# Performance work log

Measured on AMD Instinct MI355X. Metric: run time of the kernel, lower is better.

Reference implementation:

```python
import jax, jax.numpy as jnp
import numpy as np

T, B, I, H = 129, 1024, 512, 2048


def setup_inputs() -> dict:
    key = jax.random.key(0)
    ks = jax.random.split(key, 12)
    s = 1.0 / np.sqrt(H)  # torch RNNCell/Linear default U(-1/sqrt(H), 1/sqrt(H))

    def u(k, shape):
        return jax.random.uniform(k, shape, jnp.float32, -s, s)

    x = jax.random.normal(ks[0], (T, B, I), jnp.float32)
    return {
        "x": x,
        "enc_Wih": u(ks[1], (H, I)), "enc_Whh": u(ks[2], (H, H)),
        "enc_bih": u(ks[3], (H,)),   "enc_bhh": u(ks[4], (H,)),
        "dec_Wih": u(ks[5], (H, I)), "dec_Whh": u(ks[6], (H, H)),
        "dec_bih": u(ks[7], (H,)),   "dec_bhh": u(ks[8], (H,)),
        "ro_W": u(ks[9], (I, H)),    "ro_b": u(ks[10], (I,)),
    }


def reference(x, enc_Wih, enc_Whh, enc_bih, enc_bhh,
              dec_Wih, dec_Whh, dec_bih, dec_bhh, ro_W, ro_b):
    T_, B_, I_ = x.shape
    H_ = enc_Whh.shape[0]
    k = (T_ - 3) // 2

    # ---- encode: k+2 RNNCell steps over x[0:k+2] ----
    def enc_step(h, xt):
        h = jnp.tanh(xt @ enc_Wih.T + enc_bih + h @ enc_Whh.T + enc_bhh)
        return h, None

    h0 = jnp.zeros((B_, H_), x.dtype)
    h, _ = jax.lax.scan(enc_step, h0, x[:k + 2])

    # begin_char: one-hot at index 0 (also the default fill of `outputs`)
    begin = jnp.zeros((B_, I_), x.dtype).at[:, 0].set(1.0)

    # ---- decode: k+1 steps, input is zeros (so zeros @ dec_Wih == 0) ----
    def dec_step(carry, _):
        h, done = carry
        h = jnp.tanh(dec_bih + h @ dec_Whh.T + dec_bhh)
        out = jax.nn.log_softmax(h @ ro_W.T + ro_b, axis=1)  # [B, I]
        z = (jnp.argmax(out, axis=1) == 2).astype(x.dtype)
        done = jnp.maximum(done, z)
        b = done[:, None]
        o = (1.0 - b) * out + b * begin
        return (h, done), o

    done0 = jnp.zeros((B_,), x.dtype)
    (_, _), outputs = jax.lax.scan(dec_step, (h, done0), None, length=k + 1)
    return outputs  # [k+1, B, I]
```

## Files before the change

kernel.cpp:

```cpp
#include <hip/hip_runtime.h>
#include <math.h>

constexpr int Bsz  = 1024;
constexpr int Isz  = 512;
constexpr int Hsz  = 2048;
constexpr int Tenc = 65;
constexpr int Tdec = 64;
constexpr int BI   = Bsz * Isz;
constexpr int MNh  = Bsz * Hsz;

typedef _Float16 half8 __attribute__((ext_vector_type(8)));
typedef float    f32x4 __attribute__((ext_vector_type(4)));
typedef unsigned int uint;
typedef unsigned short ushort;

__device__ inline uint pack_split(float v) {
    _Float16 a0 = (_Float16)v;
    float r = (v - (float)a0) * 4096.f;
    _Float16 a1 = (_Float16)r;
    return ((uint)__builtin_bit_cast(ushort, a1) << 16) | __builtin_bit_cast(ushort, a0);
}
__device__ inline void split_pair(float v0, float v1, uint& lo, uint& hi) {
    _Float16 a0 = (_Float16)v0, a1 = (_Float16)v1;
    _Float16 b0 = (_Float16)((v0 - (float)a0) * 4096.f);
    _Float16 b1 = (_Float16)((v1 - (float)a1) * 4096.f);
    lo = (uint)__builtin_bit_cast(ushort, a0) | ((uint)__builtin_bit_cast(ushort, a1) << 16);
    hi = (uint)__builtin_bit_cast(ushort, b0) | ((uint)__builtin_bit_cast(ushort, b1) << 16);
}

struct U8 { uint4 a, b; };
__device__ inline U8 ld8(const uint* __restrict__ p) {
    U8 r; r.a = *(const uint4*)p; r.b = *(const uint4*)(p + 4); return r;
}

__device__ inline void split8(const U8& v, half8& lo, half8& hi) {
    union { uint4 u; float f[4]; } A, B;
    A.u = v.a; B.u = v.b;
    float x[8] = {A.f[0], A.f[1], A.f[2], A.f[3], B.f[0], B.f[1], B.f[2], B.f[3]};
#pragma unroll
    for (int e = 0; e < 8; ++e) {
        _Float16 a0 = (_Float16)x[e];
        float r = (x[e] - (float)a0) * 4096.f;
        lo[e] = a0; hi[e] = (_Float16)r;
    }
}
__device__ inline void unpack8(const U8& v, half8& lo, half8& hi) {
    union { uint u[4]; half8 h; } L, H;
    uint w[8] = {v.a.x, v.a.y, v.a.z, v.a.w, v.b.x, v.b.y, v.b.z, v.b.w};
#pragma unroll
    for (int q = 0; q < 4; ++q) {
        L.u[q] = __builtin_amdgcn_perm(w[2*q+1], w[2*q], 0x05040100u);
        H.u[q] = __builtin_amdgcn_perm(w[2*q+1], w[2*q], 0x07060302u);
    }
    lo = L.h; hi = H.h;
}

__device__ __forceinline__ void gll16(const uint* g, uint* l) {
    __builtin_amdgcn_global_load_lds(
        (const __attribute__((address_space(1))) void*)(uintptr_t)g,
        (__attribute__((address_space(3))) void*)(unsigned int)(uintptr_t)l,
        16, 0, 0);
}

__device__ __forceinline__ void gemm_body(
    uint* ldsA, uint* ldsB,
    const uint* A1, int K1, const uint* B1,
    const uint* A2, int K2, const uint* B2,
    float* P, int M, int N, int GM, int GN, int KS, int bid)
{
    constexpr int NV = 8;
    const int tid  = threadIdx.x;
    const int wid  = tid >> 6, lane = tid & 63;
    const int wr   = wid >> 1, wc = wid & 1;
    const int kq   = lane >> 4, lr = lane & 15;

    const int xcd = bid & 7, g = bid >> 3;
    int n_b, m_b, ks;
    const int spx = GN >> 3;
    if (spx > 0) {
        n_b = xcd * spx + (g % spx);
        int r = g / spx; m_b = r % GM; ks = r / GM;
    } else {
        const int xpn = 8 / GN;
        n_b = xcd / xpn;
        int r = g * xpn + (xcd % xpn); m_b = r % GM; ks = r / GM;
    }
    const int m0 = m_b * 128, n0 = n_b * 128;

    int offA1[4], offA2[4], offB1[4], offB2[4];
#pragma unroll
    for (int q = 0; q < 4; ++q) {
        int U = q * 256 + tid, row = U >> 3, us = U & 7;
        int u = us ^ (row & 7);
        offA1[q] = (m0 + row) * K1 + u * 4;
        offA2[q] = (m0 + row) * K2 + u * 4;
        offB1[q] = (n0 + row) * K1 + u * 4;
        offB2[q] = (n0 + row) * K2 + u * 4;
    }
    const int ldsbase = wid * 256;

    const int R1 = K1 / 32;
    const int R  = (K1 + K2) / 32;
    const int nr = R / KS;
    const int r0 = ks * nr;

    auto STAGE = [&](int r, int bi) {
        uint* Ab = ldsA + bi * 4096;
        uint* Bb = ldsB + bi * 4096;
        const bool ph1 = r < R1;
        const int kl = (ph1 ? r : r - R1) * 32;
        const uint* As = ph1 ? A1 : A2;
        const uint* Bs = ph1 ? B1 : B2;
#pragma unroll
        for (int q = 0; q < 4; ++q)
            gll16(As + (ph1 ? offA1[q] : offA2[q]) + kl, Ab + q * 1024 + ldsbase);
#pragma unroll
        for (int q = 0; q < 4; ++q)
            gll16(Bs + (ph1 ? offB1[q] : offB2[q]) + kl, Bb + q * 1024 + ldsbase);
    };

    f32x4 acc0[4][4] = {}; f32x4 acc1[4][4] = {};

    auto FRAG = [&](const uint* buf, int row, half8& lo, half8& hi) {
        const int b = row * 8, s = row & 7;
        lo = *(const half8*)(buf + (b + (kq ^ s)) * 4);
        hi = *(const half8*)(buf + (b + ((kq + 4) ^ s)) * 4);
    };

    auto COMPUTE = [&](int bi) {
        const uint* Ab = ldsA + bi * 4096;
        const uint* Bb = ldsB + bi * 4096;
        half8 a0[4], a1[4];
#pragma unroll
        for (int i = 0; i < 4; ++i) FRAG(Ab, wr * 64 + i * 16 + lr, a0[i], a1[i]);
#pragma unroll
        for (int j = 0; j < 4; ++j) {
            half8 b0, b1;
            FRAG(Bb, wc * 64 + j * 16 + lr, b0, b1);
#pragma unroll
            for (int i = 0; i < 4; ++i) {
                acc0[i][j] = __builtin_amdgcn_mfma_f32_16x16x32_f16(a0[i], b0, acc0[i][j], 0, 0, 0);
                acc1[i][j] = __builtin_amdgcn_mfma_f32_16x16x32_f16(a1[i], b0, acc1[i][j], 0, 0, 0);
                acc1[i][j] = __builtin_amdgcn_mfma_f32_16x16x32_f16(a0[i], b1, acc1[i][j], 0, 0, 0);
            }
        }
    };

    STAGE(r0, 0);
    if (nr > 1) STAGE(r0 + 1, 1);
    __builtin_amdgcn_sched_barrier(0);
    if (nr > 1) asm volatile("s_waitcnt vmcnt(%0)" :: "i"(NV) : "memory");
    else        asm volatile("s_waitcnt vmcnt(0)"  ::: "memory");
    __builtin_amdgcn_s_barrier();
    __builtin_amdgcn_sched_barrier(0);

    int bi = 0;
    for (int t = 0; t < nr; ++t) {
        COMPUTE(bi);
        if (t + 1 < nr) {
            __builtin_amdgcn_sched_barrier(0);
            __builtin_amdgcn_s_barrier();
            __builtin_amdgcn_sched_barrier(0);
            if (t + 2 < nr) {
                STAGE(r0 + t + 2, bi);
                __builtin_amdgcn_sched_barrier(0);
                asm volatile("s_waitcnt vmcnt(%0)" :: "i"(NV) : "memory");
            } else {
                asm volatile("s_waitcnt vmcnt(0)" ::: "memory");
            }
            __builtin_amdgcn_s_barrier();
            __builtin_amdgcn_sched_barrier(0);
            bi ^= 1;
        }
    }

    float* Pk = P + (size_t)ks * M * N;
#pragma unroll
    for (int j = 0; j < 4; ++j) {
        const int n = n0 + wc * 64 + j * 16 + lr;
#pragma unroll
        for (int i = 0; i < 4; ++i) {
            const int mb = m0 + wr * 64 + i * 16 + kq * 4;
#pragma unroll
            for (int r = 0; r < 4; ++r)
                Pk[(size_t)(mb + r) * N + n] = acc0[i][j][r] + 0x1p-12f * acc1[i][j][r];
        }
    }
}

__global__ __launch_bounds__(256, 2) void gemm_pk4(
    const uint* __restrict__ A1, int K1, const uint* __restrict__ B1,
    const uint* __restrict__ A2, int K2, const uint* __restrict__ B2,
    float* __restrict__ P, int M, int N, int GM, int GN, int KS)
{
    __shared__ uint ldsA[2 * 4096];
    __shared__ uint ldsB[2 * 4096];
    gemm_body(ldsA, ldsB, A1, K1, B1, A2, K2, B2, P, M, N, GM, GN, KS, blockIdx.x);
}

__global__ __launch_bounds__(256, 2) void dec_work(
    const uint* __restrict__ hcur, const uint* __restrict__ pdWhh,
    const uint* __restrict__ proW,
    float* __restrict__ hparts, float* __restrict__ ropar, int doH)
{
    __shared__ uint ldsA[2 * 4096];
    __shared__ uint ldsB[2 * 4096];
    const int bid = blockIdx.x;
    if (bid < 512) {
        if (!doH) return;
        gemm_body(ldsA, ldsB, nullptr, 0, nullptr, hcur, Hsz, pdWhh,
                  hparts, Bsz, Hsz, 8, 16, 4, bid);
    } else {
        gemm_body(ldsA, ldsB, nullptr, 0, nullptr, hcur, Hsz, proW,
                  ropar, Bsz, Isz, 8, 4, 4, bid - 512);
    }
}

__device__ __forceinline__ void combine_dev(
    const float* __restrict__ P, const float* __restrict__ b1,
    const float* __restrict__ b2, uint* __restrict__ hout, int cb)
{
    const int i0 = (cb * 256 + threadIdx.x) * 8;
    float s[8];
#pragma unroll
    for (int e = 0; e < 8; ++e) s[e] = 0.f;
#pragma unroll
    for (int p = 0; p < 4; ++p) {
        float4 a = *(const float4*)(P + (size_t)p * MNh + i0);
        float4 b = *(const float4*)(P + (size_t)p * MNh + i0 + 4);
        s[0] += a.x; s[1] += a.y; s[2] += a.z; s[3] += a.w;
        s[4] += b.x; s[5] += b.y; s[6] += b.z; s[7] += b.w;
    }
    const int n = i0 & (Hsz - 1);
    float t[8];
#pragma unroll
    for (int e = 0; e < 8; ++e) t[e] = tanhf(s[e] + b1[n + e] + b2[n + e]);
    uint lo4[4], hi4[4];
#pragma unroll
    for (int q = 0; q < 4; ++q) split_pair(t[2*q], t[2*q+1], lo4[q], hi4[q]);
    uint* base = hout + ((i0 >> 5) << 5);
    const int eo = (i0 & 31) >> 1;
    *(uint4*)(base + eo)      = *(uint4*)lo4;
    *(uint4*)(base + 16 + eo) = *(uint4*)hi4;
}

__global__ __launch_bounds__(256) void combine_h4(
    const float* __restrict__ P, const float* __restrict__ b1,
    const float* __restrict__ b2, uint* __restrict__ hout)
{
    combine_dev(P, b1, b2, hout, blockIdx.x);
}

template<int NPART>
__device__ __forceinline__ void softmax_dev(
    const float* __restrict__ parts, const float* __restrict__ rob,
    float* __restrict__ done, float* __restrict__ out, int b)
{
    const int tid = threadIdx.x;
    const size_t S = (size_t)BI;
    const float* row = parts + (size_t)b * Isz;

    float v0, v1;
    if (NPART == 1) { v0 = row[tid]; v1 = row[tid + 256]; }
    else {
        v0 = rob[tid]; v1 = rob[tid + 256];
#pragma unroll
        for (int p = 0; p < NPART; ++p) { v0 += row[p*S + tid]; v1 += row[p*S + tid + 256]; }
    }

    float mv; int mi;
    if (v0 >= v1) { mv = v0; mi = tid; } else { mv = v1; mi = tid + 256; }
#pragma unroll
    for (int off = 32; off; off >>= 1) {
        float ov = __shfl_xor(mv, off);
        int   oi = __shfl_xor(mi, off);
        if (ov > mv || (ov == mv && oi < mi)) { mv = ov; mi = oi; }
    }
    __shared__ float smv[4];
    __shared__ int   smi[4];
    __shared__ float sdone;
    const int wid = tid >> 6, lane = tid & 63;
    if (lane == 0) { smv[wid] = mv; smi[wid] = mi; }
    __syncthreads();
    if (tid == 0) {
        for (int w = 1; w < 4; ++w)
            if (smv[w] > smv[0] || (smv[w] == smv[0] && smi[w] < smi[0])) {
                smv[0] = smv[w]; smi[0] = smi[w];
            }
        float z = (smi[0] == 2) ? 1.f : 0.f;
        float dn = fmaxf(done[b], z);
        done[b] = dn;
        sdone = dn;
    }
    __syncthreads();
    mv = smv[0];

    float s = expf(v0 - mv) + expf(v1 - mv);
#pragma unroll
    for (int off = 32; off; off >>= 1) s += __shfl_xor(s, off);
    __shared__ float ssum[4];
    if (lane == 0) ssum[wid] = s;
    __syncthreads();
    if (tid == 0) ssum[0] = ssum[0] + ssum[1] + ssum[2] + ssum[3];
    __syncthreads();
    const float ls = logf(ssum[0]);

    float* orow = out + (size_t)b * Isz;
    if (sdone > 0.5f) {
        orow[tid]       = (tid == 0) ? 1.f : 0.f;
        orow[tid + 256] = 0.f;
    } else {
        orow[tid]       = v0 - mv - ls;
        orow[tid + 256] = v1 - mv - ls;
    }
}

__global__ __launch_bounds__(256) void dec_fin(
    const float* __restrict__ hparts, const float* __restrict__ dbih,
    const float* __restrict__ dbhh, uint* __restrict__ hout,
    const float* __restrict__ ropar, const float* __restrict__ rob,
    float* __restrict__ done, float* __restrict__ out, int doH)
{
    const int bid = blockIdx.x;
    if (bid < 1024) {
        if (doH) combine_dev(hparts, dbih, dbhh, hout, bid);
    } else {
        softmax_dev<4>(ropar, rob, done, out, bid - 1024);
    }
}

__global__ __launch_bounds__(256) void logsoftmax_done1(
    const float* __restrict__ logits, const float* __restrict__ rob,
    float* __restrict__ done, float* __restrict__ out)
{
    softmax_dev<1>(logits, rob, done, out, blockIdx.x);
}

__global__ __launch_bounds__(256) void split_pack2_k(
    const float* __restrict__ s, uint* __restrict__ d, int n)
{
    for (int i = blockIdx.x * 256 + threadIdx.x; i < n; i += gridDim.x * 256) {
        const int c = i >> 5, j = i & 31;
        const int kb = c << 5;
        uint v;
        if (j < 16) {
            const int k = kb + (j << 1);
            _Float16 a0 = (_Float16)s[k], a1 = (_Float16)s[k + 1];
            v = (uint)__builtin_bit_cast(ushort, a0) |
                ((uint)__builtin_bit_cast(ushort, a1) << 16);
        } else {
            const int k = kb + ((j - 16) << 1);
            float f0 = s[k], f1 = s[k + 1];
            _Float16 b0 = (_Float16)((f0 - (float)(_Float16)f0) * 4096.f);
            _Float16 b1 = (_Float16)((f1 - (float)(_Float16)f1) * 4096.f);
            v = (uint)__builtin_bit_cast(ushort, b0) |
                ((uint)__builtin_bit_cast(ushort, b1) << 16);
        }
        d[i] = v;
    }
}

#define SWZ(row, kk) (((row) * 4 + ((kk) ^ (((row) >> 1) & 3))) * 8)

template<int BM, int BN, int WR, int WC, int MP, int NP, bool TANH, bool PACKOUT>
__global__ __launch_bounds__(WR*WC*64) void gemm_sp(
    const float* __restrict__ A1, int K1, const void* __restrict__ B1,
    const uint*  __restrict__ A2, int K2, const void* __restrict__ B2,
    int b_f32,
    const float* __restrict__ bias1, const float* __restrict__ bias2,
    void* __restrict__ C, int M, int N)
{
    constexpr int NT  = WR * WC * 64;
    constexpr int AUP = BM * 4 / NT;
    constexpr int BUP = BN * 4 / NT;

    __shared__ __align__(16) _Float16 As0[BM*32], As1[BM*32];
    __shared__ __align__(16) _Float16 Bs0[BN*32], Bs1[BN*32];

    const int tid  = threadIdx.x;
    const int wid  = tid >> 6, lane = tid & 63;
    const int wrow = wid / WC, wcol = wid % WC;
    const int kq   = lane >> 4, lr = lane & 15;
    const int m0   = blockIdx.y * BM;
    const int n0   = blockIdx.x * BN;

    int aum[AUP], auk[AUP]; _Float16 *aw0[AUP], *aw1[AUP];
#pragma unroll
    for (int p = 0; p < AUP; ++p) {
        int u = tid + p * NT; aum[p] = u >> 2; auk[p] = u & 3;
        int o = SWZ(aum[p], auk[p]); aw0[p] = As0 + o; aw1[p] = As1 + o;
    }
    int bun[BUP], buk[BUP]; _Float16 *bw0[BUP], *bw1[BUP];
#pragma unroll
    for (int p = 0; p < BUP; ++p) {
        int u = tid + p * NT; bun[p] = u >> 2; buk[p] = u & 3;
        int o = SWZ(bun[p], buk[p]); bw0[p] = Bs0 + o; bw1[p] = Bs1 + o;
    }
    int aoff[MP], boff[NP];
#pragma unroll
    for (int i = 0; i < MP; ++i) { int m = wrow*(MP*16) + i*16 + lr; aoff[i] = SWZ(m, kq); }
#pragma unroll
    for (int j = 0; j < NP; ++j) { int n = wcol*(NP*16) + j*16 + lr; boff[j] = SWZ(n, kq); }

    f32x4 acc0[MP][NP] = {}; f32x4 acc1[MP][NP] = {};

    const int R = (K1 + K2) / 32;

    auto issue = [&](int rd, U8* aR, U8* bR) {
        const bool ph1 = (rd * 32) < K1;
        const int  kl  = ph1 ? rd * 32 : rd * 32 - K1;
        const int  Ka  = ph1 ? K1 : K2;
        const uint* Ap = ph1 ? (const uint*)A1 : A2;
        const uint* Bp = (const uint*)(ph1 ? B1 : B2);
#pragma unroll
        for (int p = 0; p < AUP; ++p)
            aR[p] = ld8(Ap + (size_t)(m0 + aum[p]) * Ka + kl + auk[p] * 8);
#pragma unroll
        for (int p = 0; p < BUP; ++p)
            bR[p] = ld8(Bp + (size_t)(n0 + bun[p]) * Ka + kl + buk[p] * 8);
    };

    auto stage = [&](U8* aR, U8* bR, bool aF32) {
#pragma unroll
        for (int p = 0; p < AUP; ++p) {
            half8 lo, hi;
            if (aF32) split8(aR[p], lo, hi); else unpack8(aR[p], lo, hi);
            *(half8*)aw0[p] = lo; *(half8*)aw1[p] = hi;
        }
#pragma unroll
        for (int p = 0; p < BUP; ++p) {
            half8 lo, hi;
            if (b_f32) split8(bR[p], lo, hi); else unpack8(bR[p], lo, hi);
            *(half8*)bw0[p] = lo; *(half8*)bw1[p] = hi;
        }
    };

    auto compute = [&]() {
        half8 a0[MP], a1[MP], b0[NP], b1[NP];
#pragma unroll
        for (int i = 0; i < MP; ++i) {
            a0[i] = *(const half8*)(As0 + aoff[i]);
            a1[i] = *(const half8*)(As1 + aoff[i]);
        }
#pragma unroll
        for (int j = 0; j < NP; ++j) {
            b0[j] = *(const half8*)(Bs0 + boff[j]);
            b1[j] = *(const half8*)(Bs1 + boff[j]);
        }
#pragma unroll
        for (int i = 0; i < MP; ++i)
#pragma unroll
            for (int j = 0; j < NP; ++j) {
                acc0[i][j] = __builtin_amdgcn_mfma_f32_16x16x32_f16(a0[i], b0[j], acc0[i][j], 0, 0, 0);
                acc1[i][j] = __builtin_amdgcn_mfma_f32_16x16x32_f16(a1[i], b0[j], acc1[i][j], 0, 0, 0);
                acc1[i][j] = __builtin_amdgcn_mfma_f32_16x16x32_f16(a0[i], b1[j], acc1[i][j], 0, 0, 0);
            }
    };

    U8 aA[AUP], bA[BUP], aB[AUP], bB[BUP];
    issue(0, aA, bA);
    for (int rd = 0; rd < R; rd += 2) {
        if (rd + 1 < R) issue(rd + 1, aB, bB);
        stage(aA, bA, (rd * 32) < K1);
        __syncthreads();
        compute();
        __syncthreads();
        if (rd + 1 < R) {
            if (rd + 2 < R) issue(rd + 2, aA, bA);
            stage(aB, bB, ((rd + 1) * 32) < K1);
            __syncthreads();
            compute();
            __syncthreads();
        }
    }

#pragma unroll
    for (int j = 0; j < NP; ++j) {
        const int n = n0 + wcol*(NP*16) + j*16 + lr;
        float bb = bias1 ? bias1[n] : 0.f;
        if (bias2) bb += bias2[n];
#pragma unroll
        for (int i = 0; i < MP; ++i) {
            const int mb = m0 + wrow*(MP*16) + i*16 + kq*4;
#pragma unroll
            for (int r = 0; r < 4; ++r) {
                float val = acc0[i][j][r] + 0x1p-12f * acc1[i][j][r] + bb;
                if (TANH) val = tanhf(val);
                if (PACKOUT)
                    ((uint*)C)[(size_t)(mb + r) * N + n] = pack_split(val);
                else
                    ((float*)C)[(size_t)(mb + r) * N + n] = val;
            }
        }
    }
}

extern "C" void kernel_launch(void* const* d_in, const int* in_sizes, int n_in,
                              void* d_out, int out_size, void* d_ws, size_t ws_size,
                              hipStream_t stream)
{
    const float* x    = (const float*)d_in[0];
    const float* eWih = (const float*)d_in[1];
    const float* eWhh = (const float*)d_in[2];
    const float* ebih = (const float*)d_in[3];
    const float* ebhh = (const float*)d_in[4];
    const float* dWhh = (const float*)d_in[6];
    const float* dbih = (const float*)d_in[7];
    const float* dbhh = (const float*)d_in[8];
    const float* roW  = (const float*)d_in[9];
    const float* rob  = (const float*)d_in[10];
    float* out = (float*)d_out;

    const size_t sz_pWih = (size_t)Hsz * Isz * 4;
    const size_t sz_pWhh = (size_t)Hsz * Hsz * 4;
    const size_t sz_proW = (size_t)Isz * Hsz * 4;
    const size_t sz_h    = (size_t)MNh * 4;
    const size_t sz_hp   = (size_t)4 * MNh * 4;
    const size_t sz_rp   = (size_t)4 * BI * 4;
    const size_t sz_done = (size_t)Bsz * 4;
    const size_t sz_px2  = (size_t)Tenc * BI * 4;
    const size_t sz_slot = (size_t)BI * 4;

    const size_t base = sz_pWih + 2*sz_pWhh + sz_proW + 2*sz_h + sz_hp + sz_rp + sz_done;
    const int mode = (ws_size >= base + sz_px2) ? 2
                   : (ws_size >= base + sz_slot) ? 1 : 0;

    char* ws = (char*)d_ws;

    if (mode >= 1) {
        size_t off = 0;
        uint* pWih   = (uint*)(ws + off); off += sz_pWih;
        uint* pWhh   = (uint*)(ws + off); off += sz_pWhh;
        uint* pdWhh  = (uint*)(ws + off); off += sz_pWhh;
        uint* proW   = (uint*)(ws + off); off += sz_proW;
        uint* hA     = (uint*)(ws + off); off += sz_h;
        uint* hB     = (uint*)(ws + off); off += sz_h;
        float* hparts= (float*)(ws + off); off += sz_hp;
        float* ropar = (float*)(ws + off); off += sz_rp;
        float* done  = (float*)(ws + off); off += sz_done;
        uint* px     = (uint*)(ws + off);

        split_pack2_k<<<dim3(1024), dim3(256), 0, stream>>>(eWih, pWih,  Hsz*Isz);
        split_pack2_k<<<dim3(2048), dim3(256), 0, stream>>>(eWhh, pWhh,  Hsz*Hsz);
        split_pack2_k<<<dim3(2048), dim3(256), 0, stream>>>(dWhh, pdWhh, Hsz*Hsz);
        split_pack2_k<<<dim3(1024), dim3(256), 0, stream>>>(roW,  proW,  Isz*Hsz);
        if (mode == 2)
            split_pack2_k<<<dim3(2048), dim3(256), 0, stream>>>(x, px, Tenc*BI);

        hipMemsetAsync(hA,   0, sz_h,    stream);
        hipMemsetAsync(done, 0, sz_done, stream);

        uint* h[2] = { hA, hB };
        int cur = 0;
        for (int t = 0; t < Tenc; ++t) {
            const uint* xs;
            if (mode == 2) xs = px + (size_t)t * BI;
            else {
                split_pack2_k<<<dim3(512), dim3(256), 0, stream>>>(
                    x + (size_t)t * BI, px, BI);
                xs = px;
            }
            gemm_pk4<<<dim3(512), dim3(256), 0, stream>>>(
                xs, Isz, pWih, h[cur], Hsz, pWhh,
                hparts, Bsz, Hsz, 8, 16, 4);
            combine_h4<<<dim3(1024), dim3(256), 0, stream>>>(
                hparts, ebih, ebhh, h[cur ^ 1]);
            cur ^= 1;
        }
        gemm_pk4<<<dim3(512), dim3(256), 0, stream>>>(
            nullptr, 0, nullptr, h[cur], Hsz, pdWhh,
            hparts, Bsz, Hsz, 8, 16, 4);
        combine_h4<<<dim3(1024), dim3(256), 0, stream>>>(
            hparts, dbih, dbhh, h[cur ^ 1]);
        cur ^= 1;
        for (int t = 0; t < Tdec; ++t) {
            const int doH = (t + 1 < Tdec) ? 1 : 0;
            dec_work<<<dim3(640), dim3(256), 0, stream>>>(
                h[cur], pdWhh, proW, hparts, ropar, doH);
            dec_fin<<<dim3(2048), dim3(256), 0, stream>>>(
                hparts, dbih, dbhh, h[cur ^ 1],
                ropar, rob, done, out + (size_t)t * BI, doH);
            cur ^= 1;
        }
        return;
    }

    {
        const size_t sz_lg = (size_t)BI * 4;
        size_t off = 0;
        uint*  hA     = (uint*)(ws + off); off += sz_h;
        uint*  hB     = (uint*)(ws + off); off += sz_h;
        float* logits = (float*)(ws + off); off += sz_lg;
        float* done   = (float*)(ws + off);

        hipMemsetAsync(hA, 0, sz_h, stream);
        hipMemsetAsync(done, 0, sz_done, stream);

        uint* h[2] = { hA, hB };
        const dim3 blk(256);
        const dim3 grid_h(Hsz / 128, Bsz / 64);
        const dim3 grid_ro(Isz / 64, Bsz / 64);

        int cur = 0;
        for (int t = 0; t < Tenc; ++t) {
            gemm_sp<64, 128, 2, 2, 2, 4, true, true><<<grid_h, blk, 0, stream>>>(
                x + (size_t)t * BI, Isz, eWih,
                h[cur], Hsz, eWhh, 1,
                ebih, ebhh, h[cur ^ 1], Bsz, Hsz);
            cur ^= 1;
        }
        for (int t = 0; t < Tdec; ++t) {
            gemm_sp<64, 128, 2, 2, 2, 4, true, true><<<grid_h, blk, 0, stream>>>(
                nullptr, 0, nullptr, h[cur], Hsz, dWhh, 1,
                dbih, dbhh, h[cur ^ 1], Bsz, Hsz);
            cur ^= 1;
            gemm_sp<64, 64, 2, 2, 2, 2, false, false><<<grid_ro, blk, 0, stream>>>(
                nullptr, 0, nullptr, h[cur], Hsz, roW, 1,
                rob, nullptr, logits, Bsz, Isz);
            logsoftmax_done1<<<dim3(Bsz), dim3(256), 0, stream>>>(
                logits, rob, done, out + (size_t)t * BI);
        }
    }
}
```

Baseline: 6.220 ms.

## Fuse split-K reduction and tanh into GEMM via last-arriver atomic counter

Removes the separate combine kernel for the hidden-state update. Each GEMM tile block writes its split-K partial, then bumps an atomic counter for its output tile. The fourth block to arrive reads all four partials with cache-bypassing loads, then applies the bias, tanh and the fp16 split packing in place. This cuts a kernel launch and a full pass over the partials per step. The cost is a serialized tail in the last-arriving block and correctness that depends on memory ordering and visibility across workgroups.

```diff
diff --git a/kernel.cpp b/kernel.cpp
--- a/kernel.cpp
+++ b/kernel.cpp
@@ -62,11 +62,19 @@
         16, 0, 0);
 }
 
+__device__ __forceinline__ float4 ldc4(const float* p) {
+    float4 v;
+    asm volatile("global_load_dwordx4 %0, %1, off sc0" : "=&v"(v) : "v"(p));
+    return v;
+}
+
+template<bool REDUCE>
 __device__ __forceinline__ void gemm_body(
     uint* ldsA, uint* ldsB,
     const uint* A1, int K1, const uint* B1,
     const uint* A2, int K2, const uint* B2,
-    float* P, int M, int N, int GM, int GN, int KS, int bid)
+    float* P, int M, int N, int GM, int GN, int KS, int bid,
+    const float* bias1, const float* bias2, uint* hout, uint* cnt)
 {
     constexpr int NV = 8;
     const int tid  = threadIdx.x;
@@ -186,69 +194,86 @@
                 Pk[(size_t)(mb + r) * N + n] = acc0[i][j][r] + 0x1p-12f * acc1[i][j][r];
         }
     }
-}
-
-__global__ __launch_bounds__(256, 2) void gemm_pk4(
+
+    if (REDUCE) {
+        asm volatile("s_waitcnt vmcnt(0)" ::: "memory");
+        __syncthreads();
+        __shared__ uint sold;
+        if (tid == 0)
+            sold = __hip_atomic_fetch_add(cnt + (m_b * GN + n_b), 1u,
+                       __ATOMIC_RELAXED, __HIP_MEMORY_SCOPE_AGENT);
+        __syncthreads();
+        if ((sold & 3) == 3) {
+            for (int e = tid; e < 2048; e += 256) {
+                const int row = e >> 4;
+                const int col = (e & 15) << 3;
+                const int gm = m0 + row, gn = n0 + col;
+                const size_t idx = (size_t)gm * N + gn;
+                float4 va[4], vb[4];
+#pragma unroll
+                for (int p = 0; p < 4; ++p) {
+                    va[p] = ldc4(P + (size_t)p * M * N + idx);
+                    vb[p] = ldc4(P + (size_t)p * M * N + idx + 4);
+                }
+                asm volatile("s_waitcnt vmcnt(0)" ::: "memory");
+                __builtin_amdgcn_sched_barrier(0);
+                float t8[8];
+                t8[0] = va[0].x + va[1].x + va[2].x + va[3].x;
+                t8[1] = va[0].y + va[1].y + va[2].y + va[3].y;
+                t8[2] = va[0].z + va[1].z + va[2].z + va[3].z;
+                t8[3] = va[0].w + va[1].w + va[2].w + va[3].w;
+                t8[4] = vb[0].x + vb[1].x + vb[2].x + vb[3].x;
+                t8[5] = vb[0].y + vb[1].y + vb[2].y + vb[3].y;
+                t8[6] = vb[0].z + vb[1].z + vb[2].z + vb[3].z;
+                t8[7] = vb[0].w + vb[1].w + vb[2].w + vb[3].w;
+#pragma unroll
+                for (int q = 0; q < 8; ++q)
+                    t8[q] = tanhf(t8[q] + bias1[gn + q] + bias2[gn + q]);
+                uint lo4[4], hi4[4];
+#pragma unroll
+                for (int q = 0; q < 4; ++q)
+                    split_pair(t8[2*q], t8[2*q+1], lo4[q], hi4[q]);
+                uint* base = hout + (size_t)gm * N + (gn & ~31);
+                const int eo = (gn & 31) >> 1;
+                *(uint4*)(base + eo)      = *(uint4*)lo4;
+                *(uint4*)(base + 16 + eo) = *(uint4*)hi4;
+            }
+        }
+    }
+}
+
+__global__ __launch_bounds__(256, 2) void gemm_red(
     const uint* __restrict__ A1, int K1, const uint* __restrict__ B1,
     const uint* __restrict__ A2, int K2, const uint* __restrict__ B2,
-    float* __restrict__ P, int M, int N, int GM, int GN, int KS)
+    float* __restrict__ P, int M, int N, int GM, int GN, int KS,
+    const float* __restrict__ b1, const float* __restrict__ b2,
+    uint* __restrict__ hout, uint* __restrict__ cnt)
 {
     __shared__ uint ldsA[2 * 4096];
     __shared__ uint ldsB[2 * 4096];
-    gemm_body(ldsA, ldsB, A1, K1, B1, A2, K2, B2, P, M, N, GM, GN, KS, blockIdx.x);
+    gemm_body<true>(ldsA, ldsB, A1, K1, B1, A2, K2, B2,
+                    P, M, N, GM, GN, KS, blockIdx.x, b1, b2, hout, cnt);
 }
 
 __global__ __launch_bounds__(256, 2) void dec_work(
     const uint* __restrict__ hcur, const uint* __restrict__ pdWhh,
     const uint* __restrict__ proW,
-    float* __restrict__ hparts, float* __restrict__ ropar, int doH)
+    float* __restrict__ hparts, float* __restrict__ ropar,
+    const float* __restrict__ dbih, const float* __restrict__ dbhh,
+    uint* __restrict__ hout, uint* __restrict__ cnt, int doH)
 {
     __shared__ uint ldsA[2 * 4096];
     __shared__ uint ldsB[2 * 4096];
     const int bid = blockIdx.x;
     if (bid < 512) {
         if (!doH) return;
-        gemm_body(ldsA, ldsB, nullptr, 0, nullptr, hcur, Hsz, pdWhh,
-                  hparts, Bsz, Hsz, 8, 16, 4, bid);
+        gemm_body<true>(ldsA, ldsB, nullptr, 0, nullptr, hcur, Hsz, pdWhh,
+                        hparts, Bsz, Hsz, 8, 16, 4, bid, dbih, dbhh, hout, cnt);
     } else {
-        gemm_body(ldsA, ldsB, nullptr, 0, nullptr, hcur, Hsz, proW,
-                  ropar, Bsz, Isz, 8, 4, 4, bid - 512);
-    }
-}
-
-__device__ __forceinline__ void combine_dev(
-    const float* __restrict__ P, const float* __restrict__ b1,
-    const float* __restrict__ b2, uint* __restrict__ hout, int cb)
-{
-    const int i0 = (cb * 256 + threadIdx.x) * 8;
-    float s[8];
-#pragma unroll
-    for (int e = 0; e < 8; ++e) s[e] = 0.f;
-#pragma unroll
-    for (int p = 0; p < 4; ++p) {
-        float4 a = *(const float4*)(P + (size_t)p * MNh + i0);
-        float4 b = *(const float4*)(P + (size_t)p * MNh + i0 + 4);
-        s[0] += a.x; s[1] += a.y; s[2] += a.z; s[3] += a.w;
-        s[4] += b.x; s[5] += b.y; s[6] += b.z; s[7] += b.w;
-    }
-    const int n = i0 & (Hsz - 1);
-    float t[8];
-#pragma unroll
-    for (int e = 0; e < 8; ++e) t[e] = tanhf(s[e] + b1[n + e] + b2[n + e]);
-    uint lo4[4], hi4[4];
-#pragma unroll
-    for (int q = 0; q < 4; ++q) split_pair(t[2*q], t[2*q+1], lo4[q], hi4[q]);
-    uint* base = hout + ((i0 >> 5) << 5);
-    const int eo = (i0 & 31) >> 1;
-    *(uint4*)(base + eo)      = *(uint4*)lo4;
-    *(uint4*)(base + 16 + eo) = *(uint4*)hi4;
-}
-
-__global__ __launch_bounds__(256) void combine_h4(
-    const float* __restrict__ P, const float* __restrict__ b1,
-    const float* __restrict__ b2, uint* __restrict__ hout)
-{
-    combine_dev(P, b1, b2, hout, blockIdx.x);
+        gemm_body<false>(ldsA, ldsB, nullptr, 0, nullptr, hcur, Hsz, proW,
+                         ropar, Bsz, Isz, 8, 4, 4, bid - 512,
+                         nullptr, nullptr, nullptr, nullptr);
+    }
 }
 
 template<int NPART>
@@ -316,17 +341,10 @@
 }
 
 __global__ __launch_bounds__(256) void dec_fin(
-    const float* __restrict__ hparts, const float* __restrict__ dbih,
-    const float* __restrict__ dbhh, uint* __restrict__ hout,
     const float* __restrict__ ropar, const float* __restrict__ rob,
-    float* __restrict__ done, float* __restrict__ out, int doH)
-{
-    const int bid = blockIdx.x;
-    if (bid < 1024) {
-        if (doH) combine_dev(hparts, dbih, dbhh, hout, bid);
-    } else {
-        softmax_dev<4>(ropar, rob, done, out, bid - 1024);
-    }
+    float* __restrict__ done, float* __restrict__ out)
+{
+    softmax_dev<4>(ropar, rob, done, out, blockIdx.x);
 }
 
 __global__ __launch_bounds__(256) void logsoftmax_done1(
@@ -518,10 +536,12 @@
     const size_t sz_hp   = (size_t)4 * MNh * 4;
     const size_t sz_rp   = (size_t)4 * BI * 4;
     const size_t sz_done = (size_t)Bsz * 4;
+    const size_t sz_cnt  = 512;
     const size_t sz_px2  = (size_t)Tenc * BI * 4;
     const size_t sz_slot = (size_t)BI * 4;
 
-    const size_t base = sz_pWih + 2*sz_pWhh + sz_proW + 2*sz_h + sz_hp + sz_rp + sz_done;
+    const size_t base = sz_pWih + 2*sz_pWhh + sz_proW + 2*sz_h + sz_hp + sz_rp
+                      + sz_done + sz_cnt;
     const int mode = (ws_size >= base + sz_px2) ? 2
                    : (ws_size >= base + sz_slot) ? 1 : 0;
 
@@ -538,6 +558,7 @@
         float* hparts= (float*)(ws + off); off += sz_hp;
         float* ropar = (float*)(ws + off); off += sz_rp;
         float* done  = (float*)(ws + off); off += sz_done;
+        uint* cnt    = (uint*)(ws + off);  off += sz_cnt;
         uint* px     = (uint*)(ws + off);
 
         split_pack2_k<<<dim3(1024), dim3(256), 0, stream>>>(eWih, pWih,  Hsz*Isz);
@@ -549,6 +570,7 @@
 
         hipMemsetAsync(hA,   0, sz_h,    stream);
         hipMemsetAsync(done, 0, sz_done, stream);
+        hipMemsetAsync(cnt,  0, sz_cnt,  stream);
 
         uint* h[2] = { hA, hB };
         int cur = 0;
@@ -560,26 +582,24 @@
                     x + (size_t)t * BI, px, BI);
                 xs = px;
             }
-            gemm_pk4<<<dim3(512), dim3(256), 0, stream>>>(
+            gemm_red<<<dim3(512), dim3(256), 0, stream>>>(
                 xs, Isz, pWih, h[cur], Hsz, pWhh,
-                hparts, Bsz, Hsz, 8, 16, 4);
-            combine_h4<<<dim3(1024), dim3(256), 0, stream>>>(
-                hparts, ebih, ebhh, h[cur ^ 1]);
+                hparts, Bsz, Hsz, 8, 16, 4,
+                ebih, ebhh, h[cur ^ 1], cnt);
             cur ^= 1;
         }
-        gemm_pk4<<<dim3(512), dim3(256), 0, stream>>>(
+        gemm_red<<<dim3(512), dim3(256), 0, stream>>>(
             nullptr, 0, nullptr, h[cur], Hsz, pdWhh,
-            hparts, Bsz, Hsz, 8, 16, 4);
-        combine_h4<<<dim3(1024), dim3(256), 0, stream>>>(
-            hparts, dbih, dbhh, h[cur ^ 1]);
+            hparts, Bsz, Hsz, 8, 16, 4,
+            dbih, dbhh, h[cur ^ 1], cnt);
         cur ^= 1;
         for (int t = 0; t < Tdec; ++t) {
             const int doH = (t + 1 < Tdec) ? 1 : 0;
             dec_work<<<dim3(640), dim3(256), 0, stream>>>(
-                h[cur], pdWhh, proW, hparts, ropar, doH);
-            dec_fin<<<dim3(2048), dim3(256), 0, stream>>>(
-                hparts, dbih, dbhh, h[cur ^ 1],
-                ropar, rob, done, out + (size_t)t * BI, doH);
+                h[cur], pdWhh, proW, hparts, ropar,
+                dbih, dbhh, h[cur ^ 1], cnt, doH);
+            dec_fin<<<dim3(1024), dim3(256), 0, stream>>>(
+                ropar, rob, done, out + (size_t)t * BI);
             cur ^= 1;
         }
         return;
```

Result: slower. 7.108 ms (+14.3%).
